# Kernel optimization log

Hardware: AMD Instinct MI355X
Metric: run time of the kernel (lower is better)

Reference implementation:

```python
import jax, jax.numpy as jnp
import numpy as np

N = 100000
E = 1600000
IN_FEATS, HIDDEN, NUM_CLASSES = 128, 64, 32


def _graph_conv(src, dst, x, W, b):
    """DGL GraphConv, norm='both', allow_zero_in_degree=True.
    out_i = b + sum_{(j->i)} x_j W / sqrt(max(deg_out(j),1) * max(deg_in(i),1))
    """
    ones = jnp.ones(src.shape[0], dtype=x.dtype)
    deg_out = jnp.clip(jax.ops.segment_sum(ones, src, num_segments=N), 1.0)
    deg_in = jnp.clip(jax.ops.segment_sum(ones, dst, num_segments=N), 1.0)
    # pre-normalize, apply weight first (smaller message dim), then aggregate
    h = (x * jax.lax.rsqrt(deg_out)[:, None]) @ W          # [N, out]
    agg = jax.ops.segment_sum(h[src], dst, num_segments=N)  # [N, out]
    return agg * jax.lax.rsqrt(deg_in)[:, None] + b


def setup_inputs() -> dict:
    key = jax.random.key(0)
    ks = jax.random.split(key, 8)
    x = jax.random.normal(ks[0], (N, IN_FEATS), dtype=jnp.float32)
    src1 = jax.random.randint(ks[1], (E,), 0, N, dtype=jnp.int32)
    dst1 = jax.random.randint(ks[2], (E,), 0, N, dtype=jnp.int32)
    src2 = jax.random.randint(ks[3], (E,), 0, N, dtype=jnp.int32)
    dst2 = jax.random.randint(ks[4], (E,), 0, N, dtype=jnp.int32)
    W1 = jax.random.normal(ks[5], (IN_FEATS, HIDDEN), dtype=jnp.float32) / np.sqrt(IN_FEATS)
    b1 = jnp.zeros((HIDDEN,), dtype=jnp.float32)
    W2 = jax.random.normal(ks[6], (HIDDEN, NUM_CLASSES), dtype=jnp.float32) / np.sqrt(HIDDEN)
    b2 = jnp.zeros((NUM_CLASSES,), dtype=jnp.float32)
    return {"x": x, "src1": src1, "dst1": dst1, "src2": src2, "dst2": dst2,
            "W1": W1, "b1": b1, "W2": W2, "b2": b2}


def reference(x, src1, dst1, src2, dst2, W1, b1, W2, b2):
    results = []
    for src, dst in ((src1, dst1), (src2, dst2)):
        h = jax.nn.relu(_graph_conv(src, dst, x, W1, b1))
        h = _graph_conv(src, dst, h, W2, b2)
        results.append(h)
    return jnp.mean(jnp.stack(results), axis=0)
```

## Files before the change

### kernel.cpp

```cpp
#include <hip/hip_runtime.h>

#define TPB 256
#define CAP 48
#define CHUNK 16384
#define GP1 64
#define GP2 32

__device__ inline unsigned short f2bf(float f) {
    union { float f; unsigned int u; } v; v.f = f;
    unsigned int u = v.u + 0x7FFFu + ((v.u >> 16) & 1u);
    return (unsigned short)(u >> 16);
}
__device__ inline float bf2f(unsigned short h) {
    union { unsigned int u; float f; } v; v.u = ((unsigned int)h) << 16;
    return v.f;
}
__device__ inline float bflo(unsigned int v) {
    union { unsigned int u; float f; } w; w.u = v << 16;
    return w.f;
}
__device__ inline float bfhi(unsigned int v) {
    union { unsigned int u; float f; } w; w.u = v & 0xffff0000u;
    return w.f;
}

__global__ void hist_kernel(const int* __restrict__ s1, const int* __restrict__ s2,
                            int* __restrict__ part, int E, int nchunk) {
    __shared__ int h[CHUNK];
    int b     = blockIdx.x;
    int which = b / (nchunk * GP2);
    int rem   = b % (nchunk * GP2);
    int chunk = rem / GP2;
    int p     = rem % GP2;
    const int* src = which ? s2 : s1;

    for (int i = threadIdx.x; i < CHUNK; i += TPB) h[i] = 0;
    __syncthreads();

    int lo  = chunk * CHUNK;
    int per = ((E + GP2 - 1) / GP2 + 3) & ~3;
    int e0  = p * per;
    int e1  = e0 + per; if (e1 > E) e1 = E;
    if (e0 < e1) {
        int nvec = (e1 - e0) >> 2;
        const int4* vsrc = (const int4*)(src + e0);
        for (int i = threadIdx.x; i < nvec; i += TPB) {
            int4 v = vsrc[i];
            unsigned d;
            d = (unsigned)(v.x - lo); if (d < CHUNK) atomicAdd(&h[d], 1);
            d = (unsigned)(v.y - lo); if (d < CHUNK) atomicAdd(&h[d], 1);
            d = (unsigned)(v.z - lo); if (d < CHUNK) atomicAdd(&h[d], 1);
            d = (unsigned)(v.w - lo); if (d < CHUNK) atomicAdd(&h[d], 1);
        }
        for (int e = e0 + (nvec << 2) + threadIdx.x; e < e1; e += TPB) {
            unsigned d = (unsigned)(src[e] - lo);
            if (d < CHUNK) atomicAdd(&h[d], 1);
        }
    }
    __syncthreads();
    int* dstp = part + (size_t)b * CHUNK;
    for (int i = threadIdx.x; i < CHUNK; i += TPB) dstp[i] = h[i];
}

__global__ void histreduce_kernel(const int* __restrict__ part, int* __restrict__ dout,
                                  int N, int nchunk) {
    int i = blockIdx.x * TPB + threadIdx.x;
    if (i >= 2 * N) return;
    int which = i < N ? 0 : 1;
    int node  = which ? i - N : i;
    int chunk = node / CHUNK, off = node % CHUNK;
    const int* base = part + ((size_t)(which * nchunk + chunk) * GP2) * CHUNK + off;
    int s = 0;
    #pragma unroll
    for (int p = 0; p < GP2; p++) s += base[(size_t)p * CHUNK];
    dout[i] = s;
}

__global__ void hist1_kernel(const int* __restrict__ arr, int* __restrict__ part, int E) {
    __shared__ int h[CHUNK];
    int b     = blockIdx.x;
    int chunk = b / GP1;
    int p     = b % GP1;
    for (int i = threadIdx.x; i < CHUNK; i += TPB) h[i] = 0;
    __syncthreads();
    int lo  = chunk * CHUNK;
    int per = ((E + GP1 - 1) / GP1 + 3) & ~3;
    int e0  = p * per;
    int e1  = e0 + per; if (e1 > E) e1 = E;
    if (e0 < e1) {
        int nvec = (e1 - e0) >> 2;
        const int4* vsrc = (const int4*)(arr + e0);
        for (int i = threadIdx.x; i < nvec; i += TPB) {
            int4 v = vsrc[i];
            unsigned d;
            d = (unsigned)(v.x - lo); if (d < CHUNK) atomicAdd(&h[d], 1);
            d = (unsigned)(v.y - lo); if (d < CHUNK) atomicAdd(&h[d], 1);
            d = (unsigned)(v.z - lo); if (d < CHUNK) atomicAdd(&h[d], 1);
            d = (unsigned)(v.w - lo); if (d < CHUNK) atomicAdd(&h[d], 1);
        }
        for (int e = e0 + (nvec << 2) + threadIdx.x; e < e1; e += TPB) {
            unsigned d = (unsigned)(arr[e] - lo);
            if (d < CHUNK) atomicAdd(&h[d], 1);
        }
    }
    __syncthreads();
    int* dstp = part + (size_t)b * CHUNK;
    for (int i = threadIdx.x; i < CHUNK; i += TPB) dstp[i] = h[i];
}

__global__ void offset_kernel(int* __restrict__ part, int* __restrict__ din, int N) {
    int n = blockIdx.x * TPB + threadIdx.x;
    if (n >= N) return;
    int c = n / CHUNK, o = n % CHUNK;
    int* base = part + ((size_t)c * GP1) * CHUNK + o;
    int run = n * CAP;
    #pragma unroll
    for (int p = 0; p < GP1; p++) {
        int t = base[(size_t)p * CHUNK];
        base[(size_t)p * CHUNK] = run;
        run += t;
    }
    din[n] = run - n * CAP;
}

__global__ void scatterC_kernel(const int* __restrict__ src, const int* __restrict__ dst,
                                const int* __restrict__ part, int* __restrict__ esrc, int E) {
    __shared__ int cur[CHUNK];
    int b     = blockIdx.x;
    int chunk = b / GP1;
    int p     = b % GP1;
    const int* offp = part + (size_t)b * CHUNK;
    for (int i = threadIdx.x; i < CHUNK; i += TPB) cur[i] = offp[i];
    __syncthreads();
    int lo  = chunk * CHUNK;
    int per = ((E + GP1 - 1) / GP1 + 3) & ~3;
    int e0  = p * per;
    int e1  = e0 + per; if (e1 > E) e1 = E;
    if (e0 < e1) {
        int nvec = (e1 - e0) >> 2;
        const int4* d4 = (const int4*)(dst + e0);
        const int4* s4 = (const int4*)(src + e0);
        for (int i = threadIdx.x; i < nvec; i += TPB) {
            int4 d = d4[i];
            int4 s = s4[i];
            unsigned u; int pos;
            u = (unsigned)(d.x - lo);
            if (u < CHUNK) { pos = atomicAdd(&cur[u], 1); if (pos < (lo + (int)u + 1) * CAP) esrc[pos] = s.x; }
            u = (unsigned)(d.y - lo);
            if (u < CHUNK) { pos = atomicAdd(&cur[u], 1); if (pos < (lo + (int)u + 1) * CAP) esrc[pos] = s.y; }
            u = (unsigned)(d.z - lo);
            if (u < CHUNK) { pos = atomicAdd(&cur[u], 1); if (pos < (lo + (int)u + 1) * CAP) esrc[pos] = s.z; }
            u = (unsigned)(d.w - lo);
            if (u < CHUNK) { pos = atomicAdd(&cur[u], 1); if (pos < (lo + (int)u + 1) * CAP) esrc[pos] = s.w; }
        }
        for (int e = e0 + (nvec << 2) + threadIdx.x; e < e1; e += TPB) {
            int dd = dst[e];
            unsigned u = (unsigned)(dd - lo);
            if (u < CHUNK) { int pos = atomicAdd(&cur[u], 1); if (pos < (dd + 1) * CAP) esrc[pos] = src[e]; }
        }
    }
}

__global__ void gemm1_kernel(const float* __restrict__ x, const float* __restrict__ W,
                             const int* __restrict__ dout1, const int* __restrict__ dout2,
                             unsigned short* __restrict__ Y0, unsigned short* __restrict__ Y1,
                             int N) {
    __shared__ float xs[64 * 128];
    __shared__ float ws[128 * 64];
    int tid  = threadIdx.x;
    int row0 = blockIdx.x * 64;
    for (int i = tid; i < 2048; i += TPB)
        ((float4*)ws)[i] = ((const float4*)W)[i];
    for (int i = tid; i < 2048; i += TPB) {
        int r = row0 + (i >> 5);
        ((float4*)xs)[i] = (r < N) ? ((const float4*)x)[(size_t)r * 32 + (i & 31)]
                                   : make_float4(0.f, 0.f, 0.f, 0.f);
    }
    __syncthreads();
    int tr = tid >> 4, tc = tid & 15;
    float acc[4][4] = {};
    for (int k4 = 0; k4 < 32; k4++) {
        float4 a[4], b[4];
        #pragma unroll
        for (int j = 0; j < 4; j++) a[j] = ((float4*)xs)[(tr * 4 + j) * 32 + k4];
        #pragma unroll
        for (int j = 0; j < 4; j++) b[j] = ((float4*)ws)[(k4 * 4 + j) * 16 + tc];
        #pragma unroll
        for (int i = 0; i < 4; i++) {
            float4 ai = a[i];
            acc[i][0] += ai.x * b[0].x + ai.y * b[1].x + ai.z * b[2].x + ai.w * b[3].x;
            acc[i][1] += ai.x * b[0].y + ai.y * b[1].y + ai.z * b[2].y + ai.w * b[3].y;
            acc[i][2] += ai.x * b[0].z + ai.y * b[1].z + ai.z * b[2].z + ai.w * b[3].z;
            acc[i][3] += ai.x * b[0].w + ai.y * b[1].w + ai.z * b[2].w + ai.w * b[3].w;
        }
    }
    #pragma unroll
    for (int i = 0; i < 4; i++) {
        int r = row0 + tr * 4 + i;
        if (r < N) {
            int g0 = dout1[r], g1 = dout2[r];
            float s0 = rsqrtf((float)(g0 > 1 ? g0 : 1));
            float s1 = rsqrtf((float)(g1 > 1 ? g1 : 1));
            size_t o = (size_t)r * 64 + tc * 4;
            ushort4 p0 = make_ushort4(f2bf(acc[i][0] * s0), f2bf(acc[i][1] * s0),
                                      f2bf(acc[i][2] * s0), f2bf(acc[i][3] * s0));
            ushort4 p1 = make_ushort4(f2bf(acc[i][0] * s1), f2bf(acc[i][1] * s1),
                                      f2bf(acc[i][2] * s1), f2bf(acc[i][3] * s1));
            *(ushort4*)(Y0 + o) = p0;
            *(ushort4*)(Y1 + o) = p1;
        }
    }
}

__global__ void agg1f_kernel(const int* __restrict__ esrc, const int* __restrict__ din,
                             const unsigned short* __restrict__ Yg,
                             const float* __restrict__ b1, const float* __restrict__ W2,
                             const int* __restrict__ doutg,
                             unsigned short* __restrict__ H2, int N) {
    __shared__ float hs[4][64];
    int tid  = threadIdx.x;
    int w    = tid >> 6;
    int lane = tid & 63;
    int half = lane >> 5;
    int l    = lane & 31;

    float4 w2r[8];
    #pragma unroll
    for (int k4 = 0; k4 < 8; k4++) {
        int k = (half << 5) + (k4 << 2);
        w2r[k4].x = W2[(k + 0) * 32 + l];
        w2r[k4].y = W2[(k + 1) * 32 + l];
        w2r[k4].z = W2[(k + 2) * 32 + l];
        w2r[k4].w = W2[(k + 3) * 32 + l];
    }

    int node = blockIdx.x * 4 + w;
    if (node >= N) return;

    int dn = din[node];
    float si = rsqrtf((float)(dn > 1 ? dn : 1));
    if (dn > CAP) dn = CAP;
    const int* es = esrc + (size_t)node * CAP;

    float a0 = 0.f, a1 = 0.f;
    int i = 0;
    for (; i + 8 <= dn; i += 8) {
        int4 a = *(const int4*)(es + i);
        int4 b = *(const int4*)(es + i + 4);
        int s0 = half ? a.y : a.x;
        int s1 = half ? a.w : a.z;
        int s2 = half ? b.y : b.x;
        int s3 = half ? b.w : b.z;
        unsigned v0 = *(const unsigned*)(Yg + (size_t)s0 * 64 + 2 * l);
        unsigned v1 = *(const unsigned*)(Yg + (size_t)s1 * 64 + 2 * l);
        unsigned v2 = *(const unsigned*)(Yg + (size_t)s2 * 64 + 2 * l);
        unsigned v3 = *(const unsigned*)(Yg + (size_t)s3 * 64 + 2 * l);
        a0 += bflo(v0) + bflo(v1) + bflo(v2) + bflo(v3);
        a1 += bfhi(v0) + bfhi(v1) + bfhi(v2) + bfhi(v3);
    }
    for (int e = i + half; e < dn; e += 2) {
        unsigned v = *(const unsigned*)(Yg + (size_t)es[e] * 64 + 2 * l);
        a0 += bflo(v);
        a1 += bfhi(v);
    }
    a0 += __shfl_xor(a0, 32);
    a1 += __shfl_xor(a1, 32);

    if (half == 0) {
        float2 bb = *(const float2*)(b1 + 2 * l);
        float h0 = a0 * si + bb.x; h0 = h0 > 0.f ? h0 : 0.f;
        float h1 = a1 * si + bb.y; h1 = h1 > 0.f ? h1 : 0.f;
        *(float2*)&hs[w][2 * l] = make_float2(h0, h1);
    }

    const float4* hrow = (const float4*)(hs[w] + (half << 5));
    float part = 0.f;
    #pragma unroll
    for (int k4 = 0; k4 < 8; k4++) {
        float4 hv = hrow[k4];
        part += hv.x * w2r[k4].x + hv.y * w2r[k4].y + hv.z * w2r[k4].z + hv.w * w2r[k4].w;
    }
    float total = part + __shfl_xor(part, 32);
    if (half == 0) {
        int g = doutg[node];
        float so = rsqrtf((float)(g > 1 ? g : 1));
        H2[(size_t)node * 32 + l] = f2bf(total * so);
    }
}

__global__ void agg2_kernel(const int* __restrict__ esrc, const int* __restrict__ din,
                            const unsigned short* __restrict__ H2,
                            const float* __restrict__ b2, float* __restrict__ out,
                            int N, int first) {
    int node = blockIdx.x * 16 + (threadIdx.x >> 4);
    int l    = threadIdx.x & 15;
    if (node >= N) return;
    int dn = din[node];
    float si = rsqrtf((float)(dn > 1 ? dn : 1));
    if (dn > CAP) dn = CAP;
    const int* es = esrc + (size_t)node * CAP;
    float a0 = 0.f, a1 = 0.f;
    int i = 0;
    for (; i + 8 <= dn; i += 8) {
        int4 a = *(const int4*)(es + i);
        int4 b = *(const int4*)(es + i + 4);
        unsigned v0 = *(const unsigned*)(H2 + (size_t)a.x * 32 + 2 * l);
        unsigned v1 = *(const unsigned*)(H2 + (size_t)a.y * 32 + 2 * l);
        unsigned v2 = *(const unsigned*)(H2 + (size_t)a.z * 32 + 2 * l);
        unsigned v3 = *(const unsigned*)(H2 + (size_t)a.w * 32 + 2 * l);
        unsigned v4 = *(const unsigned*)(H2 + (size_t)b.x * 32 + 2 * l);
        unsigned v5 = *(const unsigned*)(H2 + (size_t)b.y * 32 + 2 * l);
        unsigned v6 = *(const unsigned*)(H2 + (size_t)b.z * 32 + 2 * l);
        unsigned v7 = *(const unsigned*)(H2 + (size_t)b.w * 32 + 2 * l);
        a0 += bflo(v0) + bflo(v1) + bflo(v2) + bflo(v3)
            + bflo(v4) + bflo(v5) + bflo(v6) + bflo(v7);
        a1 += bfhi(v0) + bfhi(v1) + bfhi(v2) + bfhi(v3)
            + bfhi(v4) + bfhi(v5) + bfhi(v6) + bfhi(v7);
    }
    if (i + 4 <= dn) {
        int4 a = *(const int4*)(es + i);
        unsigned v0 = *(const unsigned*)(H2 + (size_t)a.x * 32 + 2 * l);
        unsigned v1 = *(const unsigned*)(H2 + (size_t)a.y * 32 + 2 * l);
        unsigned v2 = *(const unsigned*)(H2 + (size_t)a.z * 32 + 2 * l);
        unsigned v3 = *(const unsigned*)(H2 + (size_t)a.w * 32 + 2 * l);
        a0 += bflo(v0) + bflo(v1) + bflo(v2) + bflo(v3);
        a1 += bfhi(v0) + bfhi(v1) + bfhi(v2) + bfhi(v3);
        i += 4;
    }
    for (; i < dn; i++) {
        unsigned v = *(const unsigned*)(H2 + (size_t)es[i] * 32 + 2 * l);
        a0 += bflo(v);
        a1 += bfhi(v);
    }
    float2 bb = *(const float2*)(b2 + 2 * l);
    float v0 = 0.5f * (a0 * si + bb.x);
    float v1 = 0.5f * (a1 * si + bb.y);
    size_t o = (size_t)node * 32 + 2 * l;
    if (first) {
        *(float2*)(out + o) = make_float2(v0, v1);
    } else {
        float2 prev = *(const float2*)(out + o);
        *(float2*)(out + o) = make_float2(prev.x + v0, prev.y + v1);
    }
}

extern "C" void kernel_launch(void* const* d_in, const int* in_sizes, int n_in,
                              void* d_out, int out_size, void* d_ws, size_t ws_size,
                              hipStream_t stream) {
    const float* x    = (const float*)d_in[0];
    const int* srcs[2] = {(const int*)d_in[1], (const int*)d_in[3]};
    const int* dsts[2] = {(const int*)d_in[2], (const int*)d_in[4]};
    const float* W1   = (const float*)d_in[5];
    const float* b1   = (const float*)d_in[6];
    const float* W2   = (const float*)d_in[7];
    const float* b2   = (const float*)d_in[8];
    float* out        = (float*)d_out;

    const int N = in_sizes[0] / 128;
    const int E = in_sizes[1];
    const int nchunk = (N + CHUNK - 1) / CHUNK;

    unsigned short* Y1G0 = (unsigned short*)d_ws;
    unsigned short* Y1G1 = Y1G0 + (size_t)64 * N;
    float* SCR           = (float*)(Y1G1 + (size_t)64 * N);
    unsigned short* H2   = (unsigned short*)(SCR + (size_t)64 * N);
    int* DOUT            = (int*)(H2 + (size_t)32 * N);
    int* DIN             = DOUT + (size_t)2 * N;
    int* ESRC            = DIN + (size_t)2 * N;
    int* PART2           = (int*)d_ws;
    int* PART1           = (int*)SCR;

    hist_kernel<<<2 * nchunk * GP2, TPB, 0, stream>>>(srcs[0], srcs[1], PART2, E, nchunk);
    histreduce_kernel<<<(2 * N + TPB - 1) / TPB, TPB, 0, stream>>>(PART2, DOUT, N, nchunk);

    gemm1_kernel<<<(N + 63) / 64, TPB, 0, stream>>>(x, W1, DOUT, DOUT + N, Y1G0, Y1G1, N);

    for (int g = 0; g < 2; g++) {
        const unsigned short* Yg = g == 0 ? Y1G0 : Y1G1;
        int* din = DIN + (size_t)g * N;

        hist1_kernel<<<nchunk * GP1, TPB, 0, stream>>>(dsts[g], PART1, E);
        offset_kernel<<<(N + TPB - 1) / TPB, TPB, 0, stream>>>(PART1, din, N);
        scatterC_kernel<<<nchunk * GP1, TPB, 0, stream>>>(srcs[g], dsts[g], PART1, ESRC, E);

        agg1f_kernel<<<(N + 3) / 4, TPB, 0, stream>>>(ESRC, din, Yg, b1, W2,
                                                      DOUT + (size_t)g * N, H2, N);
        agg2_kernel<<<(N + 15) / 16, TPB, 0, stream>>>(ESRC, din, H2, b2, out, N, g == 0);
    }
}
```

Before: 368.1 us.

## Bucket-sort per-node edge lists by source chunk and unroll gathers to 16

```diff
diff --git a/kernel.cpp b/kernel.cpp
--- a/kernel.cpp
+++ b/kernel.cpp
@@ -3,6 +3,7 @@
 #define TPB 256
 #define CAP 48
 #define CHUNK 16384
+#define CSH 14
 #define GP1 64
 #define GP2 32
 
@@ -10,10 +11,6 @@
     union { float f; unsigned int u; } v; v.f = f;
     unsigned int u = v.u + 0x7FFFu + ((v.u >> 16) & 1u);
     return (unsigned short)(u >> 16);
-}
-__device__ inline float bf2f(unsigned short h) {
-    union { unsigned int u; float f; } v; v.u = ((unsigned int)h) << 16;
-    return v.f;
 }
 __device__ inline float bflo(unsigned int v) {
     union { unsigned int u; float f; } w; w.u = v << 16;
@@ -161,6 +158,32 @@
     }
 }
 
+__global__ void bsort_kernel(int* __restrict__ esrc, const int* __restrict__ din,
+                             int N, int nchunk) {
+    __shared__ int lb[TPB * (CAP + 1)];
+    int t = threadIdx.x;
+    int base = blockIdx.x * TPB;
+    int nn = N - base; if (nn > TPB) nn = TPB;
+    if (nn <= 0) return;
+    int total = nn * CAP;
+    const int* gs = esrc + (size_t)base * CAP;
+    for (int j = t; j < total; j += TPB) lb[j + j / CAP] = gs[j];
+    __syncthreads();
+    if (t < nn) {
+        int node = base + t;
+        int dn = din[node]; if (dn > CAP) dn = CAP;
+        const int* mb = lb + t * (CAP + 1);
+        int* eo = esrc + (size_t)node * CAP;
+        int w = 0;
+        for (int c = 0; c < nchunk; c++) {
+            for (int i = 0; i < dn; i++) {
+                int s = mb[i];
+                if ((s >> CSH) == c) eo[w++] = s;
+            }
+        }
+    }
+}
+
 __global__ void gemm1_kernel(const float* __restrict__ x, const float* __restrict__ W,
                              const int* __restrict__ dout1, const int* __restrict__ dout2,
                              unsigned short* __restrict__ Y0, unsigned short* __restrict__ Y1,
@@ -244,6 +267,32 @@
 
     float a0 = 0.f, a1 = 0.f;
     int i = 0;
+    for (; i + 16 <= dn; i += 16) {
+        int4 a = *(const int4*)(es + i);
+        int4 b = *(const int4*)(es + i + 4);
+        int4 c = *(const int4*)(es + i + 8);
+        int4 d = *(const int4*)(es + i + 12);
+        int s0 = half ? a.y : a.x;
+        int s1 = half ? a.w : a.z;
+        int s2 = half ? b.y : b.x;
+        int s3 = half ? b.w : b.z;
+        int s4 = half ? c.y : c.x;
+        int s5 = half ? c.w : c.z;
+        int s6 = half ? d.y : d.x;
+        int s7 = half ? d.w : d.z;
+        unsigned v0 = *(const unsigned*)(Yg + (size_t)s0 * 64 + 2 * l);
+        unsigned v1 = *(const unsigned*)(Yg + (size_t)s1 * 64 + 2 * l);
+        unsigned v2 = *(const unsigned*)(Yg + (size_t)s2 * 64 + 2 * l);
+        unsigned v3 = *(const unsigned*)(Yg + (size_t)s3 * 64 + 2 * l);
+        unsigned v4 = *(const unsigned*)(Yg + (size_t)s4 * 64 + 2 * l);
+        unsigned v5 = *(const unsigned*)(Yg + (size_t)s5 * 64 + 2 * l);
+        unsigned v6 = *(const unsigned*)(Yg + (size_t)s6 * 64 + 2 * l);
+        unsigned v7 = *(const unsigned*)(Yg + (size_t)s7 * 64 + 2 * l);
+        a0 += bflo(v0) + bflo(v1) + bflo(v2) + bflo(v3)
+            + bflo(v4) + bflo(v5) + bflo(v6) + bflo(v7);
+        a1 += bfhi(v0) + bfhi(v1) + bfhi(v2) + bfhi(v3)
+            + bfhi(v4) + bfhi(v5) + bfhi(v6) + bfhi(v7);
+    }
     for (; i + 8 <= dn; i += 8) {
         int4 a = *(const int4*)(es + i);
         int4 b = *(const int4*)(es + i + 4);
@@ -301,7 +350,37 @@
     const int* es = esrc + (size_t)node * CAP;
     float a0 = 0.f, a1 = 0.f;
     int i = 0;
-    for (; i + 8 <= dn; i += 8) {
+    for (; i + 16 <= dn; i += 16) {
+        int4 a = *(const int4*)(es + i);
+        int4 b = *(const int4*)(es + i + 4);
+        int4 c = *(const int4*)(es + i + 8);
+        int4 d = *(const int4*)(es + i + 12);
+        unsigned v0 = *(const unsigned*)(H2 + (size_t)a.x * 32 + 2 * l);
+        unsigned v1 = *(const unsigned*)(H2 + (size_t)a.y * 32 + 2 * l);
+        unsigned v2 = *(const unsigned*)(H2 + (size_t)a.z * 32 + 2 * l);
+        unsigned v3 = *(const unsigned*)(H2 + (size_t)a.w * 32 + 2 * l);
+        unsigned v4 = *(const unsigned*)(H2 + (size_t)b.x * 32 + 2 * l);
+        unsigned v5 = *(const unsigned*)(H2 + (size_t)b.y * 32 + 2 * l);
+        unsigned v6 = *(const unsigned*)(H2 + (size_t)b.z * 32 + 2 * l);
+        unsigned v7 = *(const unsigned*)(H2 + (size_t)b.w * 32 + 2 * l);
+        unsigned v8 = *(const unsigned*)(H2 + (size_t)c.x * 32 + 2 * l);
+        unsigned v9 = *(const unsigned*)(H2 + (size_t)c.y * 32 + 2 * l);
+        unsigned va = *(const unsigned*)(H2 + (size_t)c.z * 32 + 2 * l);
+        unsigned vb = *(const unsigned*)(H2 + (size_t)c.w * 32 + 2 * l);
+        unsigned vc = *(const unsigned*)(H2 + (size_t)d.x * 32 + 2 * l);
+        unsigned vd = *(const unsigned*)(H2 + (size_t)d.y * 32 + 2 * l);
+        unsigned ve = *(const unsigned*)(H2 + (size_t)d.z * 32 + 2 * l);
+        unsigned vf = *(const unsigned*)(H2 + (size_t)d.w * 32 + 2 * l);
+        a0 += bflo(v0) + bflo(v1) + bflo(v2) + bflo(v3)
+            + bflo(v4) + bflo(v5) + bflo(v6) + bflo(v7)
+            + bflo(v8) + bflo(v9) + bflo(va) + bflo(vb)
+            + bflo(vc) + bflo(vd) + bflo(ve) + bflo(vf);
+        a1 += bfhi(v0) + bfhi(v1) + bfhi(v2) + bfhi(v3)
+            + bfhi(v4) + bfhi(v5) + bfhi(v6) + bfhi(v7)
+            + bfhi(v8) + bfhi(v9) + bfhi(va) + bfhi(vb)
+            + bfhi(vc) + bfhi(vd) + bfhi(ve) + bfhi(vf);
+    }
+    if (i + 8 <= dn) {
         int4 a = *(const int4*)(es + i);
         int4 b = *(const int4*)(es + i + 4);
         unsigned v0 = *(const unsigned*)(H2 + (size_t)a.x * 32 + 2 * l);
@@ -316,6 +395,7 @@
             + bflo(v4) + bflo(v5) + bflo(v6) + bflo(v7);
         a1 += bfhi(v0) + bfhi(v1) + bfhi(v2) + bfhi(v3)
             + bfhi(v4) + bfhi(v5) + bfhi(v6) + bfhi(v7);
+        i += 8;
     }
     if (i + 4 <= dn) {
         int4 a = *(const int4*)(es + i);
@@ -382,6 +462,7 @@
         hist1_kernel<<<nchunk * GP1, TPB, 0, stream>>>(dsts[g], PART1, E);
         offset_kernel<<<(N + TPB - 1) / TPB, TPB, 0, stream>>>(PART1, din, N);
         scatterC_kernel<<<nchunk * GP1, TPB, 0, stream>>>(srcs[g], dsts[g], PART1, ESRC, E);
+        bsort_kernel<<<(N + TPB - 1) / TPB, TPB, 0, stream>>>(ESRC, din, N, nchunk);
 
         agg1f_kernel<<<(N + 3) / 4, TPB, 0, stream>>>(ESRC, din, Yg, b1, W2,
                                                       DOUT + (size_t)g * N, H2, N);
```

Measured after the change: 416.8 us. 1.13x slower.
